# Optimization experiments

Hardware: AMD Instinct MI355X
Metric: run time of the kernel (lower is better)

The kernel has to match this reference:

```python
import jax, jax.numpy as jnp
import numpy as np

L, H, D, A, T = 2, 8, 512, 64, 256  # layers, heads, model_dim, attention_dim, target_dim
B, S = 2, 2048
EPS = 1e-5


def _ln(x, g, b):
    m = jnp.mean(x, axis=-1, keepdims=True)
    v = jnp.mean((x - m) ** 2, axis=-1, keepdims=True)
    return (x - m) / jnp.sqrt(v + EPS) * g + b


def setup_inputs() -> dict:
    key = jax.random.key(0)
    ks = jax.random.split(key, 16)
    s = 0.02
    inp = {
        "x": jax.random.normal(ks[0], (B, S, D), jnp.float32),
        # per-head QKV projections, stacked over layers and heads
        "Wq": jax.random.normal(ks[1], (L, H, D, A), jnp.float32) * s,
        "bq": jnp.zeros((L, H, A), jnp.float32),
        "Wk": jax.random.normal(ks[2], (L, H, D, A), jnp.float32) * s,
        "bk": jnp.zeros((L, H, A), jnp.float32),
        "Wv": jax.random.normal(ks[3], (L, H, D, A), jnp.float32) * s,
        "bv": jnp.zeros((L, H, A), jnp.float32),
        # output projection of concatenated heads: [H*A, D]
        "Wo": jax.random.normal(ks[4], (L, H * A, D), jnp.float32) * s,
        "bo": jnp.zeros((L, D), jnp.float32),
        # AddNorm after attention
        "ln1_g": jnp.ones((L, D), jnp.float32),
        "ln1_b": jnp.zeros((L, D), jnp.float32),
        # FFN (hidden_dim == model_dim in this module)
        "W1": jax.random.normal(ks[5], (L, D, D), jnp.float32) * s,
        "b1": jnp.zeros((L, D), jnp.float32),
        "W2": jax.random.normal(ks[6], (L, D, D), jnp.float32) * s,
        "b2": jnp.zeros((L, D), jnp.float32),
        # AddNorm after FFN
        "ln2_g": jnp.ones((L, D), jnp.float32),
        "ln2_b": jnp.zeros((L, D), jnp.float32),
        # final projection to target_dim
        "Wp": jax.random.normal(ks[7], (D, T), jnp.float32) * s,
        "bp": jnp.zeros((T,), jnp.float32),
    }
    return inp


def reference(x, Wq, bq, Wk, bk, Wv, bv, Wo, bo, ln1_g, ln1_b,
              W1, b1, W2, b2, ln2_g, ln2_b, Wp, bp):
    scale = 1.0 / jnp.sqrt(jnp.asarray(A, x.dtype))
    for i in range(L):
        # batched per-head QKV projections (math identical to per-head Linears)
        q = jnp.einsum('bsd,hda->bhsa', x, Wq[i]) + bq[i][:, None, :]
        k = jnp.einsum('bsd,hda->bhsa', x, Wk[i]) + bk[i][:, None, :]
        v = jnp.einsum('bsd,hda->bhsa', x, Wv[i]) + bv[i][:, None, :]
        scores = jnp.einsum('bhsa,bhta->bhst', q, k) * scale  # [B,H,S,S]
        attn = jax.nn.softmax(scores, axis=-1)
        heads = jnp.einsum('bhst,bhta->bhsa', attn, v)        # [B,H,S,A]
        concat = heads.transpose(0, 2, 1, 3).reshape(x.shape[0], x.shape[1], H * A)
        mha = concat @ Wo[i] + bo[i]
        x = _ln(x + mha, ln1_g[i], ln1_b[i])
        ffn = jax.nn.relu(x @ W1[i] + b1[i]) @ W2[i] + b2[i]
        x = _ln(x + ffn, ln2_g[i], ln2_b[i])
    return x @ Wp + bp
```

## Files before the change

### kernel.cpp

```cpp
#include <hip/hip_runtime.h>
#include <hip/hip_bf16.h>

#define MDIM 4096
#define DDIM 512
#define ADIM 64
#define HHEADS 8
#define SLEN 2048
#define TDIM 256
#define SPLIT 8

typedef __attribute__((ext_vector_type(8))) short short8;
typedef __attribute__((ext_vector_type(16))) float f32x16;

__device__ __forceinline__ unsigned short f2bf(float f) {
    union { __hip_bfloat16 h; unsigned short u; } c;
    c.h = __float2bfloat16(f);
    return c.u;
}
__device__ __forceinline__ float bf2f(short s) {
    return __uint_as_float((unsigned)(unsigned short)s << 16);
}

#define N1 524288
#define N2 524288
#define NP 131072
__global__ __launch_bounds__(256) void prep_k(
    const float* __restrict__ Wq, const float* __restrict__ Wk, const float* __restrict__ Wv,
    const float* __restrict__ Wo, const float* __restrict__ W1, const float* __restrict__ W2,
    const float* __restrict__ Wp, const float* __restrict__ x,
    short* __restrict__ Wqt, short* __restrict__ Wkt, short* __restrict__ Wvt,
    short* __restrict__ Wot, short* __restrict__ W1t, short* __restrict__ W2t,
    short* __restrict__ Wpt, short* __restrict__ xbf)
{
    long idx = (long)blockIdx.x * 256 + threadIdx.x;
    if (idx < 3L * N1) {
        int t = (int)(idx / N1);
        int r = (int)(idx % N1);
        int a = r & 63, k = (r >> 6) & 511, hh = r >> 15;
        const float* src = (t == 0) ? Wq : (t == 1) ? Wk : Wv;
        short* dst = (t == 0) ? Wqt : (t == 1) ? Wkt : Wvt;
        dst[((size_t)hh << 15) + (a << 9) + k] = (short)f2bf(src[r]);
        return;
    }
    idx -= 3L * N1;
    if (idx < 3L * N2) {
        int t = (int)(idx / N2);
        int r = (int)(idx % N2);
        int n = r & 511, k = (r >> 9) & 511, i = r >> 18;
        const float* src = (t == 0) ? Wo : (t == 1) ? W1 : W2;
        short* dst = (t == 0) ? Wot : (t == 1) ? W1t : W2t;
        dst[((size_t)i << 18) + (n << 9) + k] = (short)f2bf(src[r]);
        return;
    }
    idx -= 3L * N2;
    if (idx < NP) {
        int r = (int)idx;
        int n = r & 255, k = r >> 8;
        Wpt[n * 512 + k] = (short)f2bf(Wp[r]);
        return;
    }
    idx -= NP;
    xbf[idx] = (short)f2bf(x[idx]);
}

#define LDT 66
__global__ __launch_bounds__(256, 2) void gemm_bf(
    const short* __restrict__ A, const short* __restrict__ Bt,
    const float* __restrict__ bias, void* __restrict__ Cout,
    int M, int N, int K, int flags)
{
    __shared__ short As[64 * LDT];
    __shared__ short Bs[64 * LDT];
    const int tid = threadIdx.x;
    const int wave = tid >> 6, lane = tid & 63;
    const int l31 = lane & 31, hi = lane >> 5;
    const int wm = wave >> 1, wn = wave & 1;
    const int m0 = blockIdx.y * 64, n0 = blockIdx.x * 64;

    f32x16 acc;
#pragma unroll
    for (int r = 0; r < 16; ++r) acc[r] = 0.f;

    const int sr = tid >> 2;
    const int sc = (tid & 3) * 16;

    for (int k0 = 0; k0 < K; k0 += 64) {
        __syncthreads();
        *(short8*)&As[sr * LDT + sc]     = *(const short8*)&A[(size_t)(m0 + sr) * K + k0 + sc];
        *(short8*)&As[sr * LDT + sc + 8] = *(const short8*)&A[(size_t)(m0 + sr) * K + k0 + sc + 8];
        *(short8*)&Bs[sr * LDT + sc]     = *(const short8*)&Bt[(size_t)(n0 + sr) * K + k0 + sc];
        *(short8*)&Bs[sr * LDT + sc + 8] = *(const short8*)&Bt[(size_t)(n0 + sr) * K + k0 + sc + 8];
        __syncthreads();

        short8 af[4], bfm[4];
#pragma unroll
        for (int ks = 0; ks < 4; ++ks) {
            af[ks]  = *(const short8*)&As[(wm * 32 + l31) * LDT + ks * 16 + hi * 8];
            bfm[ks] = *(const short8*)&Bs[(wn * 32 + l31) * LDT + ks * 16 + hi * 8];
        }
#pragma unroll
        for (int ks = 0; ks < 4; ++ks)
            acc = __builtin_amdgcn_mfma_f32_32x32x16_bf16(af[ks], bfm[ks], acc, 0, 0, 0);
    }

    const int col = n0 + wn * 32 + l31;
    const float bb = bias[col];
    const int rbase = m0 + wm * 32 + 4 * hi;
#pragma unroll
    for (int r = 0; r < 16; ++r) {
        int row = rbase + (r & 3) + 8 * (r >> 2);
        float v = acc[r] + bb;
        if (flags & 1) v = fmaxf(v, 0.f);
        if (flags & 2) ((short*)Cout)[(size_t)row * N + col] = (short)f2bf(v);
        else           ((float*)Cout)[(size_t)row * N + col] = v;
    }
}

#define EXPC 0.1803368801111244f

__global__ __launch_bounds__(256, 2) void qkv_bf(
    const short* __restrict__ A,
    const short* __restrict__ Wqt, const short* __restrict__ Wkt, const short* __restrict__ Wvt,
    const float* __restrict__ bq, const float* __restrict__ bk, const float* __restrict__ bv,
    short* __restrict__ Oq, short* __restrict__ Ok, short* __restrict__ Ov)
{
    __shared__ short As[128 * LDT];
    __shared__ short Bs[64 * LDT];
    const int tid = threadIdx.x;
    const int wave = tid >> 6, lane = tid & 63;
    const int l31 = lane & 31, hi = lane >> 5;
    const int wm = wave >> 1, wn = wave & 1;
    const int m0 = blockIdx.y * 128;
    const int nt = blockIdx.x;
    const int which = nt >> 3, h = nt & 7;

    const short* Bt = ((which == 0) ? Wqt : (which == 1) ? Wkt : Wvt) + (size_t)h * 64 * 512;
    const float* bias = ((which == 0) ? bq : (which == 1) ? bk : bv) + h * 64;
    short* Out = (which == 0) ? Oq : (which == 1) ? Ok : Ov;

    f32x16 acc[2];
#pragma unroll
    for (int ms = 0; ms < 2; ++ms)
#pragma unroll
        for (int r = 0; r < 16; ++r) acc[ms][r] = 0.f;

    const int sr = tid >> 3;
    const int sc = (tid & 7) * 8;

    for (int k0 = 0; k0 < 512; k0 += 64) {
        __syncthreads();
#pragma unroll
        for (int p = 0; p < 4; ++p)
            *(short8*)&As[(p * 32 + sr) * LDT + sc] =
                *(const short8*)&A[(size_t)(m0 + p * 32 + sr) * 512 + k0 + sc];
#pragma unroll
        for (int p = 0; p < 2; ++p)
            *(short8*)&Bs[(p * 32 + sr) * LDT + sc] =
                *(const short8*)&Bt[(size_t)(p * 32 + sr) * 512 + k0 + sc];
        __syncthreads();

        short8 af[2][4], bfm[4];
#pragma unroll
        for (int ms = 0; ms < 2; ++ms)
#pragma unroll
            for (int ks = 0; ks < 4; ++ks)
                af[ms][ks] = *(const short8*)&As[(wm * 64 + ms * 32 + l31) * LDT + ks * 16 + hi * 8];
#pragma unroll
        for (int ks = 0; ks < 4; ++ks)
            bfm[ks] = *(const short8*)&Bs[(wn * 32 + l31) * LDT + ks * 16 + hi * 8];
#pragma unroll
        for (int ms = 0; ms < 2; ++ms)
#pragma unroll
            for (int ks = 0; ks < 4; ++ks)
                acc[ms] = __builtin_amdgcn_mfma_f32_32x32x16_bf16(af[ms][ks], bfm[ks], acc[ms], 0, 0, 0);
    }

    const int a = wn * 32 + l31;
    const float bb = bias[a];
    const int b = m0 >> 11;
    const int sb = (m0 & (SLEN - 1)) + wm * 64;
    const int bh = b * HHEADS + h;

    if (which == 0) {
        short* Ob = Out + (size_t)bh * SLEN * 64;
#pragma unroll
        for (int ms = 0; ms < 2; ++ms)
#pragma unroll
            for (int r = 0; r < 16; ++r) {
                int s = sb + ms * 32 + (r & 3) + 8 * (r >> 2) + 4 * hi;
                Ob[(size_t)s * 64 + a] = (short)f2bf((acc[ms][r] + bb) * EXPC);
            }
    } else if (which == 1) {
        short* Ob = Out + (size_t)bh * SLEN * 64;
#pragma unroll
        for (int ms = 0; ms < 2; ++ms)
#pragma unroll
            for (int r = 0; r < 16; ++r) {
                int s = sb + ms * 32 + (r & 3) + 8 * (r >> 2) + 4 * hi;
                Ob[(size_t)s * 64 + a] = (short)f2bf(acc[ms][r] + bb);
            }
    } else {
        short* Ob = Out + ((size_t)bh * 64 + a) * SLEN;
#pragma unroll
        for (int ms = 0; ms < 2; ++ms)
#pragma unroll
            for (int g = 0; g < 4; ++g) {
                int s = sb + ms * 32 + 8 * g + 4 * hi;
                ushort4 w;
                w.x = f2bf(acc[ms][4 * g + 0] + bb);
                w.y = f2bf(acc[ms][4 * g + 1] + bb);
                w.z = f2bf(acc[ms][4 * g + 2] + bb);
                w.w = f2bf(acc[ms][4 * g + 3] + bb);
                *(ushort4*)&Ob[s] = w;
            }
    }
}

__global__ __launch_bounds__(256, 2) void attn_mfma(
    const short* __restrict__ Qb, const short* __restrict__ Kb,
    const short* __restrict__ Vtb, short* __restrict__ Op,
    float* __restrict__ lp)
{
    __shared__ short Ks[64 * 72];
    __shared__ short Vs[64 * 72];

    const int tid = threadIdx.x;
    const int wid = tid >> 6;
    const int lane = tid & 63;
    const int l31 = lane & 31;
    const int hi = lane >> 5;

    const int qt = blockIdx.x;
    const int bh = blockIdx.y;
    const int sp = blockIdx.z;

    const short* Qg = Qb + (size_t)bh * SLEN * 64;
    const short* Kg = Kb + (size_t)bh * SLEN * 64;
    const short* Vg = Vtb + (size_t)bh * 64 * SLEN;

    const int q0 = qt * 256 + wid * 64;

    short8 qf[2][4];
#pragma unroll
    for (int nt = 0; nt < 2; ++nt)
#pragma unroll
        for (int ks = 0; ks < 4; ++ks)
            qf[nt][ks] = *(const short8*)&Qg[(size_t)(q0 + nt * 32 + l31) * 64 + ks * 16 + hi * 8];

    f32x16 oacc[2][2], lacc[2];
#pragma unroll
    for (int nt = 0; nt < 2; ++nt) {
#pragma unroll
        for (int r = 0; r < 16; ++r) lacc[nt][r] = 0.f;
#pragma unroll
        for (int dt = 0; dt < 2; ++dt)
#pragma unroll
            for (int r = 0; r < 16; ++r) oacc[nt][dt][r] = 0.f;
    }

    short8 ones;
#pragma unroll
    for (int j = 0; j < 8; ++j) ones[j] = (short)0x3F80;

    const int srow = tid >> 2;
    const int sch = (tid & 3) * 16;

    for (int kt = 0; kt < SLEN / SPLIT / 64; ++kt) {
        const int k0 = sp * (SLEN / SPLIT) + kt * 64;
        __syncthreads();
        *(short8*)&Ks[srow * 72 + sch]     = *(const short8*)&Kg[(size_t)(k0 + srow) * 64 + sch];
        *(short8*)&Ks[srow * 72 + sch + 8] = *(const short8*)&Kg[(size_t)(k0 + srow) * 64 + sch + 8];
        *(short8*)&Vs[srow * 72 + sch]     = *(const short8*)&Vg[(size_t)srow * SLEN + k0 + sch];
        *(short8*)&Vs[srow * 72 + sch + 8] = *(const short8*)&Vg[(size_t)srow * SLEN + k0 + sch + 8];
        __syncthreads();

        short8 kf[2][4], vf[2][4];
#pragma unroll
        for (int mt = 0; mt < 2; ++mt)
#pragma unroll
            for (int ks = 0; ks < 4; ++ks)
                kf[mt][ks] = *(const short8*)&Ks[(mt * 32 + l31) * 72 + ks * 16 + hi * 8];
#pragma unroll
        for (int dt = 0; dt < 2; ++dt)
#pragma unroll
            for (int p = 0; p < 4; ++p)
                vf[dt][p] = *(const short8*)&Vs[(dt * 32 + l31) * 72 + p * 16 + hi * 8];

#pragma unroll
        for (int nt = 0; nt < 2; ++nt) {
            f32x16 sacc[2];
#pragma unroll
            for (int mt = 0; mt < 2; ++mt) {
                f32x16 s;
#pragma unroll
                for (int r = 0; r < 16; ++r) s[r] = 0.f;
#pragma unroll
                for (int ks = 0; ks < 4; ++ks)
                    s = __builtin_amdgcn_mfma_f32_32x32x16_bf16(kf[mt][ks], qf[nt][ks], s, 0, 0, 0);
                sacc[mt] = s;
            }

            int2 pk[2][4];
#pragma unroll
            for (int mt = 0; mt < 2; ++mt)
#pragma unroll
                for (int g = 0; g < 4; ++g) {
                    unsigned a0 = __float_as_uint(__builtin_amdgcn_exp2f(sacc[mt][4 * g + 0]));
                    unsigned a1 = __float_as_uint(__builtin_amdgcn_exp2f(sacc[mt][4 * g + 1]));
                    unsigned a2 = __float_as_uint(__builtin_amdgcn_exp2f(sacc[mt][4 * g + 2]));
                    unsigned a3 = __float_as_uint(__builtin_amdgcn_exp2f(sacc[mt][4 * g + 3]));
                    pk[mt][g].x = (int)__builtin_amdgcn_perm(a1, a0, 0x07060302u);
                    pk[mt][g].y = (int)__builtin_amdgcn_perm(a3, a2, 0x07060302u);
                }

            int2 xch[2][2];
#pragma unroll
            for (int mt = 0; mt < 2; ++mt)
#pragma unroll
                for (int h2 = 0; h2 < 2; ++h2) {
                    int2 v = hi ? pk[mt][2 * h2] : pk[mt][2 * h2 + 1];
                    xch[mt][h2].x = __shfl_xor(v.x, 32);
                    xch[mt][h2].y = __shfl_xor(v.y, 32);
                }

#pragma unroll
            for (int p = 0; p < 4; ++p) {
                const int mt = p >> 1, h2 = p & 1;
                const int ga = 2 * h2, gb = 2 * h2 + 1;
                const int2 X = xch[mt][h2];
                union { int4 i; short8 s; } u;
                u.i.x = hi ? X.x : pk[mt][ga].x;
                u.i.y = hi ? X.y : pk[mt][ga].y;
                u.i.z = hi ? pk[mt][gb].x : X.x;
                u.i.w = hi ? pk[mt][gb].y : X.y;
                lacc[nt] = __builtin_amdgcn_mfma_f32_32x32x16_bf16(u.s, ones, lacc[nt], 0, 0, 0);
#pragma unroll
                for (int dt = 0; dt < 2; ++dt)
                    oacc[nt][dt] = __builtin_amdgcn_mfma_f32_32x32x16_bf16(u.s, vf[dt][p], oacc[nt][dt], 0, 0, 0);
            }
        }
    }

#pragma unroll
    for (int nt = 0; nt < 2; ++nt) {
        if (l31 == 0) {
#pragma unroll
            for (int r = 0; r < 16; ++r) {
                int qrow = (r & 3) + 8 * (r >> 2) + 4 * hi;
                lp[((size_t)(sp * 16 + bh)) * SLEN + q0 + nt * 32 + qrow] = lacc[nt][r];
            }
        }
#pragma unroll
        for (int dt = 0; dt < 2; ++dt) {
#pragma unroll
            for (int r = 0; r < 16; ++r) {
                int qrow = (r & 3) + 8 * (r >> 2) + 4 * hi;
                size_t addr = (((size_t)(sp * 16 + bh)) * SLEN + (q0 + nt * 32 + qrow)) * 64 + dt * 32 + l31;
                Op[addr] = (short)f2bf(oacc[nt][dt][r]);
            }
        }
    }
}

__global__ __launch_bounds__(256) void merge_k(
    const short* __restrict__ Op, const float* __restrict__ lp,
    short* __restrict__ hc)
{
    const int g = blockIdx.x * 256 + threadIdx.x;
    const int d4 = g & 15;
    const int s = (g >> 4) & (SLEN - 1);
    const int bh = g >> 15;

    float o[4] = {0.f, 0.f, 0.f, 0.f};
    float ls = 0.f;
#pragma unroll
    for (int sp = 0; sp < SPLIT; ++sp) {
        const size_t base = (((size_t)(sp * 16 + bh)) * SLEN + s);
        ushort4 u4 = *(const ushort4*)&Op[base * 64 + d4 * 4];
        o[0] += bf2f((short)u4.x); o[1] += bf2f((short)u4.y);
        o[2] += bf2f((short)u4.z); o[3] += bf2f((short)u4.w);
        ls += lp[base];
    }
    const int b = bh >> 3, h = bh & 7;
    const float inv = 1.f / ls;
    ushort4 w;
    w.x = f2bf(o[0] * inv); w.y = f2bf(o[1] * inv);
    w.z = f2bf(o[2] * inv); w.w = f2bf(o[3] * inv);
    *(ushort4*)&hc[((size_t)(b * SLEN + s)) * DDIM + h * 64 + d4 * 4] = w;
}

__global__ __launch_bounds__(256) void addnorm_bf(
    short* __restrict__ X, const float* __restrict__ Y,
    const float* __restrict__ g, const float* __restrict__ beta)
{
    const int lane = threadIdx.x & 63;
    const int t = blockIdx.x * 4 + (threadIdx.x >> 6);
    short* xr = X + (size_t)t * DDIM;
    const float* yr = Y + (size_t)t * DDIM;
    const int c0 = lane * 8;

    short8 x8 = *(const short8*)&xr[c0];
    float4 y0 = *(const float4*)&yr[c0];
    float4 y1 = *(const float4*)&yr[c0 + 4];
    float v[8];
    v[0] = bf2f(x8[0]) + y0.x; v[1] = bf2f(x8[1]) + y0.y;
    v[2] = bf2f(x8[2]) + y0.z; v[3] = bf2f(x8[3]) + y0.w;
    v[4] = bf2f(x8[4]) + y1.x; v[5] = bf2f(x8[5]) + y1.y;
    v[6] = bf2f(x8[6]) + y1.z; v[7] = bf2f(x8[7]) + y1.w;

    float s1 = 0.f, s2 = 0.f;
#pragma unroll
    for (int j = 0; j < 8; ++j) { s1 += v[j]; s2 += v[j] * v[j]; }
#pragma unroll
    for (int off = 1; off < 64; off <<= 1) {
        s1 += __shfl_xor(s1, off);
        s2 += __shfl_xor(s2, off);
    }
    float mean = s1 * (1.0f / DDIM);
    float var = s2 * (1.0f / DDIM) - mean * mean;
    float rstd = rsqrtf(var + 1e-5f);

    float4 ga = *(const float4*)&g[c0];
    float4 gb = *(const float4*)&g[c0 + 4];
    float4 ba = *(const float4*)&beta[c0];
    float4 bb = *(const float4*)&beta[c0 + 4];
    float gg[8] = {ga.x, ga.y, ga.z, ga.w, gb.x, gb.y, gb.z, gb.w};
    float bt[8] = {ba.x, ba.y, ba.z, ba.w, bb.x, bb.y, bb.z, bb.w};

    short8 o8;
#pragma unroll
    for (int j = 0; j < 8; ++j)
        o8[j] = (short)f2bf((v[j] - mean) * rstd * gg[j] + bt[j]);
    *(short8*)&xr[c0] = o8;
}

extern "C" void kernel_launch(void* const* d_in, const int* in_sizes, int n_in,
                              void* d_out, int out_size, void* d_ws, size_t ws_size,
                              hipStream_t stream)
{
    (void)in_sizes; (void)n_in; (void)out_size; (void)ws_size;
    const float* x   = (const float*)d_in[0];
    const float* Wq  = (const float*)d_in[1];
    const float* bq  = (const float*)d_in[2];
    const float* Wk  = (const float*)d_in[3];
    const float* bk  = (const float*)d_in[4];
    const float* Wv  = (const float*)d_in[5];
    const float* bv  = (const float*)d_in[6];
    const float* Wo  = (const float*)d_in[7];
    const float* bo  = (const float*)d_in[8];
    const float* g1  = (const float*)d_in[9];
    const float* be1 = (const float*)d_in[10];
    const float* W1  = (const float*)d_in[11];
    const float* b1  = (const float*)d_in[12];
    const float* W2  = (const float*)d_in[13];
    const float* b2  = (const float*)d_in[14];
    const float* g2  = (const float*)d_in[15];
    const float* be2 = (const float*)d_in[16];
    const float* Wp  = (const float*)d_in[17];
    const float* bp  = (const float*)d_in[18];

    char* wsb = (char*)d_ws;
    const size_t MB = 1024 * 1024;
    short* xbf   = (short*)(wsb + 0);
    short* Qbuf  = (short*)(wsb + 4 * MB);
    short* Kbuf  = (short*)(wsb + 8 * MB);
    short* Vtbuf = (short*)(wsb + 12 * MB);
    short* hcbf  = (short*)(wsb + 16 * MB);
    float* y     = (float*)(wsb + 20 * MB);
    short* hidbf = (short*)(wsb + 28 * MB);
    short* Opart = (short*)(wsb + 32 * MB);
    float* lpart = (float*)(wsb + 64 * MB);
    short* Wqt   = (short*)(wsb + 65 * MB);
    short* Wkt   = (short*)(wsb + 66 * MB);
    short* Wvt   = (short*)(wsb + 67 * MB);
    short* Wot   = (short*)(wsb + 68 * MB);
    short* W1t   = (short*)(wsb + 69 * MB);
    short* W2t   = (short*)(wsb + 70 * MB);
    short* Wpt   = (short*)(wsb + 71 * MB);

    prep_k<<<20992, 256, 0, stream>>>(Wq, Wk, Wv, Wo, W1, W2, Wp, x,
                                      Wqt, Wkt, Wvt, Wot, W1t, W2t, Wpt, xbf);

    for (int i = 0; i < 2; ++i) {
        const size_t wOffQ = (size_t)i * 262144;
        const size_t wOffS = (size_t)i * 262144;
        qkv_bf<<<dim3(24, 32), 256, 0, stream>>>(
            xbf, Wqt + wOffQ, Wkt + wOffQ, Wvt + wOffQ,
            bq + i * 512, bk + i * 512, bv + i * 512,
            Qbuf, Kbuf, Vtbuf);
        attn_mfma<<<dim3(8, 16, SPLIT), 256, 0, stream>>>(Qbuf, Kbuf, Vtbuf, Opart, lpart);
        merge_k<<<2048, 256, 0, stream>>>(Opart, lpart, hcbf);
        gemm_bf<<<dim3(8, 64), 256, 0, stream>>>(
            hcbf, Wot + wOffS, bo + i * 512, y, MDIM, DDIM, DDIM, 0);
        addnorm_bf<<<1024, 256, 0, stream>>>(xbf, y, g1 + i * 512, be1 + i * 512);
        gemm_bf<<<dim3(8, 64), 256, 0, stream>>>(
            xbf, W1t + wOffS, b1 + i * 512, hidbf, MDIM, DDIM, DDIM, 3);
        gemm_bf<<<dim3(8, 64), 256, 0, stream>>>(
            hidbf, W2t + wOffS, b2 + i * 512, y, MDIM, DDIM, DDIM, 0);
        addnorm_bf<<<1024, 256, 0, stream>>>(xbf, y, g2 + i * 512, be2 + i * 512);
    }
    gemm_bf<<<dim3(4, 64), 256, 0, stream>>>(
        xbf, Wpt, bp, (float*)d_out, MDIM, TDIM, DDIM, 0);
}
```

Baseline: 304.2 us.

## Split-K the 512x512 GEMMs into two partials and fuse reduction into consumers

The Wo, W1 and W2 GEMMs now run with a K-split of 2 over a third grid dimension and write fp32 partial tiles. The partials are summed in the consumers: addnorm adds both partials plus the bias, and the W2 GEMM loads both W1 partials, adds the bias, applies ReLU and converts to bf16 while staging its A tile. This doubles the block count of these small GEMMs to improve occupancy, at the cost of extra fp32 partial traffic. The attention split count is also cut from 8 to 4 to reduce partial-output and merge work.

New measurement: 333.0 us. 9.5% more time.

```diff
diff --git a/kernel.cpp b/kernel.cpp
--- a/kernel.cpp
+++ b/kernel.cpp
@@ -7,7 +7,7 @@
 #define HHEADS 8
 #define SLEN 2048
 #define TDIM 256
-#define SPLIT 8
+#define SPLIT 4
 
 typedef __attribute__((ext_vector_type(8))) short short8;
 typedef __attribute__((ext_vector_type(16))) float f32x16;
@@ -65,9 +65,9 @@
 
 #define LDT 66
 __global__ __launch_bounds__(256, 2) void gemm_bf(
-    const short* __restrict__ A, const short* __restrict__ Bt,
-    const float* __restrict__ bias, void* __restrict__ Cout,
-    int M, int N, int K, int flags)
+    const void* __restrict__ Ap, const short* __restrict__ Bt,
+    const float* __restrict__ abias, const float* __restrict__ bias,
+    float* __restrict__ Cout, int M, int N, int K, int KS, int flags)
 {
     __shared__ short As[64 * LDT];
     __shared__ short Bs[64 * LDT];
@@ -76,6 +76,8 @@
     const int l31 = lane & 31, hi = lane >> 5;
     const int wm = wave >> 1, wn = wave & 1;
     const int m0 = blockIdx.y * 64, n0 = blockIdx.x * 64;
+    const int z = blockIdx.z;
+    const int kc = K / KS;
 
     f32x16 acc;
 #pragma unroll
@@ -84,10 +86,29 @@
     const int sr = tid >> 2;
     const int sc = (tid & 3) * 16;
 
-    for (int k0 = 0; k0 < K; k0 += 64) {
+    for (int k0 = z * kc; k0 < z * kc + kc; k0 += 64) {
         __syncthreads();
-        *(short8*)&As[sr * LDT + sc]     = *(const short8*)&A[(size_t)(m0 + sr) * K + k0 + sc];
-        *(short8*)&As[sr * LDT + sc + 8] = *(const short8*)&A[(size_t)(m0 + sr) * K + k0 + sc + 8];
+        if (flags & 1) {
+            const float* A0 = (const float*)Ap + (size_t)(m0 + sr) * K + k0 + sc;
+            const float* A1 = A0 + (size_t)M * K;
+            short tmp[16];
+#pragma unroll
+            for (int q = 0; q < 4; ++q) {
+                float4 a = *(const float4*)(A0 + q * 4);
+                float4 b = *(const float4*)(A1 + q * 4);
+                float4 bv = *(const float4*)(abias + k0 + sc + q * 4);
+                tmp[4 * q + 0] = (short)f2bf(fmaxf(a.x + b.x + bv.x, 0.f));
+                tmp[4 * q + 1] = (short)f2bf(fmaxf(a.y + b.y + bv.y, 0.f));
+                tmp[4 * q + 2] = (short)f2bf(fmaxf(a.z + b.z + bv.z, 0.f));
+                tmp[4 * q + 3] = (short)f2bf(fmaxf(a.w + b.w + bv.w, 0.f));
+            }
+            *(short8*)&As[sr * LDT + sc]     = *(short8*)&tmp[0];
+            *(short8*)&As[sr * LDT + sc + 8] = *(short8*)&tmp[8];
+        } else {
+            const short* A = (const short*)Ap;
+            *(short8*)&As[sr * LDT + sc]     = *(const short8*)&A[(size_t)(m0 + sr) * K + k0 + sc];
+            *(short8*)&As[sr * LDT + sc + 8] = *(const short8*)&A[(size_t)(m0 + sr) * K + k0 + sc + 8];
+        }
         *(short8*)&Bs[sr * LDT + sc]     = *(const short8*)&Bt[(size_t)(n0 + sr) * K + k0 + sc];
         *(short8*)&Bs[sr * LDT + sc + 8] = *(const short8*)&Bt[(size_t)(n0 + sr) * K + k0 + sc + 8];
         __syncthreads();
@@ -103,16 +124,14 @@
             acc = __builtin_amdgcn_mfma_f32_32x32x16_bf16(af[ks], bfm[ks], acc, 0, 0, 0);
     }
 
+    float* outp = Cout + (size_t)z * M * N;
     const int col = n0 + wn * 32 + l31;
-    const float bb = bias[col];
+    const float bb = (KS == 1) ? bias[col] : 0.f;
     const int rbase = m0 + wm * 32 + 4 * hi;
 #pragma unroll
     for (int r = 0; r < 16; ++r) {
         int row = rbase + (r & 3) + 8 * (r >> 2);
-        float v = acc[r] + bb;
-        if (flags & 1) v = fmaxf(v, 0.f);
-        if (flags & 2) ((short*)Cout)[(size_t)row * N + col] = (short)f2bf(v);
-        else           ((float*)Cout)[(size_t)row * N + col] = v;
+        outp[(size_t)row * N + col] = acc[r] + bb;
     }
 }
 
@@ -390,23 +409,33 @@
 }
 
 __global__ __launch_bounds__(256) void addnorm_bf(
-    short* __restrict__ X, const float* __restrict__ Y,
+    short* __restrict__ X, const float* __restrict__ Y0, const float* __restrict__ Y1,
+    const float* __restrict__ bvec,
     const float* __restrict__ g, const float* __restrict__ beta)
 {
     const int lane = threadIdx.x & 63;
     const int t = blockIdx.x * 4 + (threadIdx.x >> 6);
     short* xr = X + (size_t)t * DDIM;
-    const float* yr = Y + (size_t)t * DDIM;
+    const float* y0r = Y0 + (size_t)t * DDIM;
+    const float* y1r = Y1 + (size_t)t * DDIM;
     const int c0 = lane * 8;
 
     short8 x8 = *(const short8*)&xr[c0];
-    float4 y0 = *(const float4*)&yr[c0];
-    float4 y1 = *(const float4*)&yr[c0 + 4];
+    float4 a0 = *(const float4*)&y0r[c0];
+    float4 a1 = *(const float4*)&y0r[c0 + 4];
+    float4 b0 = *(const float4*)&y1r[c0];
+    float4 b1 = *(const float4*)&y1r[c0 + 4];
+    float4 c0v = *(const float4*)&bvec[c0];
+    float4 c1v = *(const float4*)&bvec[c0 + 4];
     float v[8];
-    v[0] = bf2f(x8[0]) + y0.x; v[1] = bf2f(x8[1]) + y0.y;
-    v[2] = bf2f(x8[2]) + y0.z; v[3] = bf2f(x8[3]) + y0.w;
-    v[4] = bf2f(x8[4]) + y1.x; v[5] = bf2f(x8[5]) + y1.y;
-    v[6] = bf2f(x8[6]) + y1.z; v[7] = bf2f(x8[7]) + y1.w;
+    v[0] = bf2f(x8[0]) + a0.x + b0.x + c0v.x;
+    v[1] = bf2f(x8[1]) + a0.y + b0.y + c0v.y;
+    v[2] = bf2f(x8[2]) + a0.z + b0.z + c0v.z;
+    v[3] = bf2f(x8[3]) + a0.w + b0.w + c0v.w;
+    v[4] = bf2f(x8[4]) + a1.x + b1.x + c1v.x;
+    v[5] = bf2f(x8[5]) + a1.y + b1.y + c1v.y;
+    v[6] = bf2f(x8[6]) + a1.z + b1.z + c1v.z;
+    v[7] = bf2f(x8[7]) + a1.w + b1.w + c1v.w;
 
     float s1 = 0.f, s2 = 0.f;
 #pragma unroll
@@ -466,17 +495,18 @@
     short* Kbuf  = (short*)(wsb + 8 * MB);
     short* Vtbuf = (short*)(wsb + 12 * MB);
     short* hcbf  = (short*)(wsb + 16 * MB);
-    float* y     = (float*)(wsb + 20 * MB);
-    short* hidbf = (short*)(wsb + 28 * MB);
-    short* Opart = (short*)(wsb + 32 * MB);
-    float* lpart = (float*)(wsb + 64 * MB);
-    short* Wqt   = (short*)(wsb + 65 * MB);
-    short* Wkt   = (short*)(wsb + 66 * MB);
-    short* Wvt   = (short*)(wsb + 67 * MB);
-    short* Wot   = (short*)(wsb + 68 * MB);
-    short* W1t   = (short*)(wsb + 69 * MB);
-    short* W2t   = (short*)(wsb + 70 * MB);
-    short* Wpt   = (short*)(wsb + 71 * MB);
+    float* y0    = (float*)(wsb + 20 * MB);
+    float* h0    = (float*)(wsb + 36 * MB);
+    short* Opart = (short*)(wsb + 52 * MB);
+    float* lpart = (float*)(wsb + 68 * MB);
+    short* Wqt   = (short*)(wsb + 69 * MB);
+    short* Wkt   = (short*)(wsb + 70 * MB);
+    short* Wvt   = (short*)(wsb + 71 * MB);
+    short* Wot   = (short*)(wsb + 72 * MB);
+    short* W1t   = (short*)(wsb + 73 * MB);
+    short* W2t   = (short*)(wsb + 74 * MB);
+    short* Wpt   = (short*)(wsb + 75 * MB);
+    float* y1    = y0 + (size_t)MDIM * DDIM;
 
     prep_k<<<20992, 256, 0, stream>>>(Wq, Wk, Wv, Wo, W1, W2, Wp, x,
                                       Wqt, Wkt, Wvt, Wot, W1t, W2t, Wpt, xbf);
@@ -490,15 +520,17 @@
             Qbuf, Kbuf, Vtbuf);
         attn_mfma<<<dim3(8, 16, SPLIT), 256, 0, stream>>>(Qbuf, Kbuf, Vtbuf, Opart, lpart);
         merge_k<<<2048, 256, 0, stream>>>(Opart, lpart, hcbf);
-        gemm_bf<<<dim3(8, 64), 256, 0, stream>>>(
-            hcbf, Wot + wOffS, bo + i * 512, y, MDIM, DDIM, DDIM, 0);
-        addnorm_bf<<<1024, 256, 0, stream>>>(xbf, y, g1 + i * 512, be1 + i * 512);
-        gemm_bf<<<dim3(8, 64), 256, 0, stream>>>(
-            xbf, W1t + wOffS, b1 + i * 512, hidbf, MDIM, DDIM, DDIM, 3);
-        gemm_bf<<<dim3(8, 64), 256, 0, stream>>>(
-            hidbf, W2t + wOffS, b2 + i * 512, y, MDIM, DDIM, DDIM, 0);
-        addnorm_bf<<<1024, 256, 0, stream>>>(xbf, y, g2 + i * 512, be2 + i * 512);
-    }
-    gemm_bf<<<dim3(4, 64), 256, 0, stream>>>(
-        xbf, Wpt, bp, (float*)d_out, MDIM, TDIM, DDIM, 0);
-}
+        gemm_bf<<<dim3(8, 64, 2), 256, 0, stream>>>(
+            hcbf, Wot + wOffS, nullptr, nullptr, y0, MDIM, DDIM, DDIM, 2, 0);
+        addnorm_bf<<<1024, 256, 0, stream>>>(xbf, y0, y1, bo + i * 512,
+                                             g1 + i * 512, be1 + i * 512);
+        gemm_bf<<<dim3(8, 64, 2), 256, 0, stream>>>(
+            xbf, W1t + wOffS, nullptr, nullptr, h0, MDIM, DDIM, DDIM, 2, 0);
+        gemm_bf<<<dim3(8, 64, 2), 256, 0, stream>>>(
+            h0, W2t + wOffS, b1 + i * 512, nullptr, y0, MDIM, DDIM, DDIM, 2, 1);
+        addnorm_bf<<<1024, 256, 0, stream>>>(xbf, y0, y1, b2 + i * 512,
+                                             g2 + i * 512, be2 + i * 512);
+    }
+    gemm_bf<<<dim3(4, 64, 1), 256, 0, stream>>>(
+        xbf, Wpt, nullptr, bp, (float*)d_out, MDIM, TDIM, DDIM, 1, 0);
+}
```
